# Optimization experiments

Hardware: AMD Instinct MI355X
Metric: run time of the kernel (lower is better)

## Reference

```python
import jax, jax.numpy as jnp
import numpy as np

N = 131072        # total points
M = 34            # max_num_neighbors (hard-coded in forward)
K = 15            # kernel points (torch-points3d default for 3D KPConv)
C_IN, C_OUT = 32, 64
POINT_INFLUENCE = 0.04        # prev_grid_size * sigma
KERNEL_RADIUS = 1.5 * POINT_INFLUENCE  # _INFLUENCE_TO_RADIUS * point_influence
BN_EPS = 1e-5
NEG_SLOPE = 0.2


def setup_inputs() -> dict:
    key = jax.random.key(0)
    ks = jax.random.split(key, 6)
    # points in a [0, 0.1]^3 box so random neighbors can fall inside the influence radius
    xyz = jax.random.uniform(ks[0], (N, 3), jnp.float32) * 0.1
    feats = jax.random.normal(ks[1], (N, C_IN), jnp.float32)
    neighbor_idx = jax.random.randint(ks[2], (N, M), 0, N, dtype=jnp.int32)
    # fixed kernel-point disposition: points inside a sphere of radius KERNEL_RADIUS
    kp_dir = jax.random.normal(ks[3], (K, 3), jnp.float32)
    kp_dir = kp_dir / jnp.linalg.norm(kp_dir, axis=1, keepdims=True)
    kp_rad = jax.random.uniform(ks[4], (K, 1), jnp.float32) ** (1.0 / 3.0)
    k_points = kp_dir * kp_rad * KERNEL_RADIUS
    weight = jax.random.normal(ks[5], (K, C_IN, C_OUT), jnp.float32) / np.sqrt(K * C_IN)
    gamma = jnp.ones((C_OUT,), jnp.float32)
    beta = jnp.zeros((C_OUT,), jnp.float32)
    return {"xyz": xyz, "feats": feats, "neighbor_idx": neighbor_idx,
            "weight": weight, "k_points": k_points, "gamma": gamma, "beta": beta}


def _kpconv(xyz, feats, neighbor_idx, weight, k_points):
    # shadow point / shadow feature row for out-of-range neighbor index == N
    sup = jnp.concatenate([xyz, jnp.full((1, 3), 1e6, xyz.dtype)], axis=0)
    f = jnp.concatenate([feats, jnp.zeros((1, feats.shape[1]), feats.dtype)], axis=0)
    # [N, M, 3] neighbor offsets relative to each query point
    nb = sup[neighbor_idx] - xyz[:, None, :]
    # [N, M, K] distance from each neighbor to each kernel point
    diff = nb[:, :, None, :] - k_points[None, None, :, :]
    dist = jnp.sqrt(jnp.sum(diff * diff, axis=-1))
    # linear kernel influence, 'sum' aggregation
    w = jnp.maximum(0.0, 1.0 - dist / POINT_INFLUENCE)          # [N, M, K]
    nb_f = f[neighbor_idx]                                       # [N, M, C_IN]
    wf = jnp.einsum('nmk,nmc->nkc', w, nb_f)                     # [N, K, C_IN]
    return jnp.einsum('nkc,kcd->nd', wf, weight)                 # [N, C_OUT]


def reference(xyz, feats, neighbor_idx, weight, k_points, gamma, beta):
    out = _kpconv(xyz, feats, neighbor_idx, weight, k_points)
    # FastBatchNorm1d (training-mode batch statistics) + LeakyReLU(0.2)
    mean = jnp.mean(out, axis=0)
    var = jnp.mean((out - mean) ** 2, axis=0)
    out = (out - mean) * jax.lax.rsqrt(var + BN_EPS) * gamma + beta
    return jnp.where(out >= 0, out, NEG_SLOPE * out)
```

## Files before the change

kernel.cpp:

```cpp
#include <hip/hip_runtime.h>

#define NPTS 131072
#define MNBR 34
#define KP 15
#define CIN 32
#define COUT 64
#define INV_INFL 25.0f
#define BN_EPS 1e-5f
#define NEG_SLOPE 0.2f
#define PPB 16
#define NBLK (NPTS / PPB)
#define NBIN 2048

typedef unsigned short u16;
typedef unsigned int u32;
typedef short short8 __attribute__((ext_vector_type(8)));
typedef float f32x4 __attribute__((ext_vector_type(4)));

static __device__ __forceinline__ u16 f2bf(float f) {
    u32 x = __float_as_uint(f);
    x += 0x7fffu + ((x >> 16) & 1u);
    return (u16)(x >> 16);
}
static __device__ __forceinline__ u32 pk2bf(float lo, float hi) {
    u32 a = __float_as_uint(lo) + 0x8000u;
    u32 b = __float_as_uint(hi) + 0x8000u;
    return (a >> 16) | (b & 0xffff0000u);
}

#define WS_WT   0u
#define WS_SCSH 65536u
#define WS_SP   131072u
#define WS_QP   655360u
#define WS_FB   1179648u

__global__ __launch_bounds__(256) void prep(const float* __restrict__ Wg,
                                            const float* __restrict__ feats,
                                            u16* __restrict__ WT, u32* __restrict__ FBu,
                                            float* __restrict__ SpQp) {
    int b = blockIdx.x;
    if (b < 120) {
        int tid2 = b * 256 + threadIdx.x;
        int i = tid2 >> 6, d = tid2 & 63;
        WT[d * 480 + i] = f2bf(Wg[tid2]);
    } else if (b < 120 + 8193) {
        int g = (b - 120) * 256 + threadIdx.x;
        if (g < ((NPTS + 1) * CIN) / 2) {
            int e = g * 2;
            u32 v = 0;
            if (e < NPTS * CIN)
                v = (u32)f2bf(feats[e]) | ((u32)f2bf(feats[e + 1]) << 16);
            FBu[g] = v;
        }
    } else {
        int idx = (b - 8313) * 256 + threadIdx.x;
        if (idx < 2 * 64 * NBIN) SpQp[idx] = 0.f;
    }
}

__global__ __launch_bounds__(128, 3) void kpconv_conv(
    const float* __restrict__ xyz, const int* __restrict__ nbr,
    const u16* __restrict__ FB, const u16* __restrict__ WT,
    const float* __restrict__ kpts, float* __restrict__ out,
    float* __restrict__ Sp, float* __restrict__ Qp)
{
    __shared__ u32 wf[PPB * 256];
    __shared__ u32 nbt[2][16 * 68];
    __shared__ u16 wk[2][16 * 64];

    const int tid = threadIdx.x, lane = tid & 63, wave = tid >> 6;
    const int q = lane >> 4, t = lane & 15;

    float ax[16], ay[16], az[16], ck[16];
    #pragma unroll
    for (int k = 0; k < KP; ++k) {
        float kx = kpts[3 * k], ky = kpts[3 * k + 1], kz = kpts[3 * k + 2];
        ax[k] = -2.f * kx; ay[k] = -2.f * ky; az[k] = -2.f * kz;
        ck[k] = fmaf(kx, kx, fmaf(ky, ky, kz * kz));
    }
    ax[15] = 0.f; ay[15] = 0.f; az[15] = 0.f; ck[15] = 1e12f;

    u32* nb = nbt[wave];
    u16* wl = wk[wave];
    const int pbase = blockIdx.x * PPB + wave * 8;

    int ci = NPTS;
    if (lane < MNBR) ci = nbr[(size_t)pbase * MNBR + lane];
    if ((unsigned)ci > (unsigned)NPTS) ci = NPTS;
    int nn = NPTS;
    if (lane < MNBR) nn = nbr[(size_t)(pbase + 1) * MNBR + lane];
    if ((unsigned)nn > (unsigned)NPTS) nn = NPTS;

    int il = ci < NPTS ? ci : 0;
    float cnx = xyz[3 * il], cny = xyz[3 * il + 1], cnz = xyz[3 * il + 2];
    const uint4* fr = (const uint4*)(FB + (size_t)ci * CIN);
    uint4 cf0 = fr[0], cf1 = fr[1], cf2 = fr[2], cf3 = fr[3];

    for (int p = 0; p < 8; ++p) {
        int nn2 = NPTS;
        if (p < 6) {
            if (lane < MNBR) nn2 = nbr[(size_t)(pbase + p + 2) * MNBR + lane];
            if ((unsigned)nn2 > (unsigned)NPTS) nn2 = NPTS;
        }
        float nx1 = 0.f, ny1 = 0.f, nz1 = 0.f;
        uint4 nf0 = {}, nf1 = {}, nf2 = {}, nf3 = {};
        if (p < 7) {
            int il1 = nn < NPTS ? nn : 0;
            nx1 = xyz[3 * il1]; ny1 = xyz[3 * il1 + 1]; nz1 = xyz[3 * il1 + 2];
            const uint4* fr1 = (const uint4*)(FB + (size_t)nn * CIN);
            nf0 = fr1[0]; nf1 = fr1[1]; nf2 = fr1[2]; nf3 = fr1[3];
        }

        const int n = pbase + p;
        const float qx = xyz[3 * n], qy = xyz[3 * n + 1], qz = xyz[3 * n + 2];
        float ox = cnx - qx, oy = cny - qy, oz = cnz - qz;
        if (ci >= NPTS) { ox = 1e6f; oy = 0.f; oz = 0.f; }
        const float oo = fmaf(ox, ox, fmaf(oy, oy, oz * oz));

        #pragma unroll
        for (int k = 0; k < 16; ++k) {
            float d2 = fmaf(ox, ax[k], fmaf(oy, ay[k], fmaf(oz, az[k], ck[k]))) + oo;
            float d = __builtin_amdgcn_sqrtf(d2);
            float w = fmaxf(0.f, fmaf(d, -INV_INFL, 1.f));
            wl[k * 64 + ((((lane >> 3) ^ (k & 7))) << 3) + (lane & 7)] =
                (u16)((__float_as_uint(w) + 0x8000u) >> 16);
        }

        {
            u32 fd[16] = {cf0.x, cf0.y, cf0.z, cf0.w, cf1.x, cf1.y, cf1.z, cf1.w,
                          cf2.x, cf2.y, cf2.z, cf2.w, cf3.x, cf3.y, cf3.z, cf3.w};
            #pragma unroll
            for (int w16 = 0; w16 < 16; ++w16)
                nb[w16 * 68 + lane] = fd[w16];
        }

        cnx = nx1; cny = ny1; cnz = nz1;
        cf0 = nf0; cf1 = nf1; cf2 = nf2; cf3 = nf3;
        ci = nn; nn = nn2;

        short8 a0 = *(const short8*)&wl[t * 64 + (((q) ^ (t & 7)) << 3)];
        short8 a1 = *(const short8*)&wl[t * 64 + (((4 + q) ^ (t & 7)) << 3)];

        uint4 b0 = *(const uint4*)&nb[t * 68 + 8 * q];
        uint4 b1 = *(const uint4*)&nb[t * 68 + 8 * q + 4];
        uint4 b2 = *(const uint4*)&nb[t * 68 + 8 * q + 32];
        uint4 b3 = *(const uint4*)&nb[t * 68 + 8 * q + 36];
        union { short8 v; u32 d[4]; } e0, o0, e1, o1;
        {
            u32 r0[8] = {b0.x, b0.y, b0.z, b0.w, b1.x, b1.y, b1.z, b1.w};
            u32 r1[8] = {b2.x, b2.y, b2.z, b2.w, b3.x, b3.y, b3.z, b3.w};
            #pragma unroll
            for (int i2 = 0; i2 < 4; ++i2) {
                u32 a = r0[2 * i2], b = r0[2 * i2 + 1];
                e0.d[i2] = (a & 0xffffu) | (b << 16);
                o0.d[i2] = (a >> 16) | (b & 0xffff0000u);
                a = r1[2 * i2]; b = r1[2 * i2 + 1];
                e1.d[i2] = (a & 0xffffu) | (b << 16);
                o1.d[i2] = (a >> 16) | (b & 0xffff0000u);
            }
        }

        f32x4 c0 = {0.f, 0.f, 0.f, 0.f}, c1 = {0.f, 0.f, 0.f, 0.f};
        c0 = __builtin_amdgcn_mfma_f32_16x16x32_bf16(a0, e0.v, c0, 0, 0, 0);
        c0 = __builtin_amdgcn_mfma_f32_16x16x32_bf16(a1, e1.v, c0, 0, 0, 0);
        c1 = __builtin_amdgcn_mfma_f32_16x16x32_bf16(a0, o0.v, c1, 0, 0, 0);
        c1 = __builtin_amdgcn_mfma_f32_16x16x32_bf16(a1, o1.v, c1, 0, 0, 0);

        const int row = wave * 8 + p;
        #pragma unroll
        for (int r = 0; r < 4; ++r) {
            int ko = q * 4 + r;
            u32 pk = pk2bf(c0[r], c1[r]);
            int unit = ko * 4 + (t >> 2);
            wf[row * 256 + ((unit ^ (row & 7)) << 2) + (t & 3)] = pk;
        }
    }
    __syncthreads();

    const int wcol0 = (wave * 2 + 0) * 16 + t;
    const int wcol1 = (wave * 2 + 1) * 16 + t;
    f32x4 A0 = {0.f, 0.f, 0.f, 0.f}, A1 = {0.f, 0.f, 0.f, 0.f};
    const u16* wt0 = WT + wcol0 * 480 + q * 8;
    const u16* wt1 = WT + wcol1 * 480 + q * 8;
    #pragma unroll
    for (int ks = 0; ks < KP; ++ks) {
        const int u = ks * 4 + q;
        short8 a  = *(const short8*)&wf[t * 256 + ((u ^ (t & 7)) << 2)];
        short8 bb0 = *(const short8*)(wt0 + ks * 32);
        short8 bb1 = *(const short8*)(wt1 + ks * 32);
        A0 = __builtin_amdgcn_mfma_f32_16x16x32_bf16(a, bb0, A0, 0, 0, 0);
        A1 = __builtin_amdgcn_mfma_f32_16x16x32_bf16(a, bb1, A1, 0, 0, 0);
    }
    const int base = blockIdx.x * PPB;
    float s0 = 0.f, q0 = 0.f, s1 = 0.f, q1 = 0.f;
    #pragma unroll
    for (int r = 0; r < 4; ++r) {
        float v0 = A0[r], v1 = A1[r];
        out[(base + q * 4 + r) * COUT + wcol0] = v0;
        out[(base + q * 4 + r) * COUT + wcol1] = v1;
        s0 += v0; q0 = fmaf(v0, v0, q0);
        s1 += v1; q1 = fmaf(v1, v1, q1);
    }
    s0 += __shfl_xor(s0, 16, 64); s0 += __shfl_xor(s0, 32, 64);
    q0 += __shfl_xor(q0, 16, 64); q0 += __shfl_xor(q0, 32, 64);
    s1 += __shfl_xor(s1, 16, 64); s1 += __shfl_xor(s1, 32, 64);
    q1 += __shfl_xor(q1, 16, 64); q1 += __shfl_xor(q1, 32, 64);
    if (q == 0) {
        const int bin = blockIdx.x >> 2;
        atomicAdd(&Sp[wcol0 * NBIN + bin], s0);
        atomicAdd(&Qp[wcol0 * NBIN + bin], q0);
        atomicAdd(&Sp[wcol1 * NBIN + bin], s1);
        atomicAdd(&Qp[wcol1 * NBIN + bin], q1);
    }
}

__global__ __launch_bounds__(256) void bn_reduce(
    const float* __restrict__ Sp, const float* __restrict__ Qp,
    const float* __restrict__ gamma, const float* __restrict__ beta,
    float* __restrict__ scsh)
{
    const int ch = blockIdx.x;
    const float4* S4 = (const float4*)(Sp + ch * NBIN);
    const float4* Q4 = (const float4*)(Qp + ch * NBIN);
    float s = 0.f, qq = 0.f;
    #pragma unroll
    for (int r = 0; r < NBIN / 4 / 256; ++r) {
        float4 a = S4[threadIdx.x + 256 * r]; s  += a.x + a.y + a.z + a.w;
        float4 b = Q4[threadIdx.x + 256 * r]; qq += b.x + b.y + b.z + b.w;
    }
    #pragma unroll
    for (int off = 1; off < 64; off <<= 1) {
        s += __shfl_xor(s, off, 64); qq += __shfl_xor(qq, off, 64);
    }
    __shared__ float red[8];
    const int w = threadIdx.x >> 6;
    if ((threadIdx.x & 63) == 0) { red[w * 2] = s; red[w * 2 + 1] = qq; }
    __syncthreads();
    if (threadIdx.x == 0) {
        s  = red[0] + red[2] + red[4] + red[6];
        qq = red[1] + red[3] + red[5] + red[7];
        float mean = s * (1.0f / NPTS);
        float var  = qq * (1.0f / NPTS) - mean * mean;
        float sc = gamma[ch] * rsqrtf(var + BN_EPS);
        scsh[ch] = sc;
        scsh[64 + ch] = beta[ch] - mean * sc;
    }
}

__global__ __launch_bounds__(256) void bn_apply(
    float* __restrict__ out, const float* __restrict__ scsh)
{
    __shared__ float sc[64], sh[64];
    const int tid = threadIdx.x;
    if (tid < 64) { sc[tid] = scsh[tid]; sh[tid] = scsh[64 + tid]; }
    __syncthreads();
    const int gid = blockIdx.x * 256 + tid;
    float4 v = ((const float4*)out)[gid];
    const int c0 = (gid * 4) & 63;
    float y0 = fmaf(v.x, sc[c0 + 0], sh[c0 + 0]);
    float y1 = fmaf(v.y, sc[c0 + 1], sh[c0 + 1]);
    float y2 = fmaf(v.z, sc[c0 + 2], sh[c0 + 2]);
    float y3 = fmaf(v.w, sc[c0 + 3], sh[c0 + 3]);
    float4 w;
    w.x = fmaxf(y0, NEG_SLOPE * y0);
    w.y = fmaxf(y1, NEG_SLOPE * y1);
    w.z = fmaxf(y2, NEG_SLOPE * y2);
    w.w = fmaxf(y3, NEG_SLOPE * y3);
    ((float4*)out)[gid] = w;
}

extern "C" void kernel_launch(void* const* d_in, const int* in_sizes, int n_in,
                              void* d_out, int out_size, void* d_ws, size_t ws_size,
                              hipStream_t stream) {
    (void)in_sizes; (void)n_in; (void)out_size; (void)ws_size;
    const float* xyz   = (const float*)d_in[0];
    const float* feats = (const float*)d_in[1];
    const int*   nbr   = (const int*)d_in[2];
    const float* Wg    = (const float*)d_in[3];
    const float* kpts  = (const float*)d_in[4];
    const float* gamma = (const float*)d_in[5];
    const float* beta  = (const float*)d_in[6];
    float* out = (float*)d_out;
    char* ws = (char*)d_ws;
    u16*   WT   = (u16*)(ws + WS_WT);
    float* scsh = (float*)(ws + WS_SCSH);
    float* Sp   = (float*)(ws + WS_SP);
    float* Qp   = (float*)(ws + WS_QP);
    u16*   FB   = (u16*)(ws + WS_FB);

    prep<<<dim3(120 + 8193 + 1024), dim3(256), 0, stream>>>(Wg, feats, WT, (u32*)FB, Sp);
    kpconv_conv<<<dim3(NBLK), dim3(128), 0, stream>>>(xyz, nbr, FB, WT, kpts, out, Sp, Qp);
    bn_reduce<<<dim3(64), dim3(256), 0, stream>>>(Sp, Qp, gamma, beta, scsh);
    bn_apply<<<dim3((NPTS * COUT) / (256 * 4)), dim3(256), 0, stream>>>(out, scsh);
}
```

Baseline: 248.0 us.

## Restructure neighbor gather and kernel-weight compute to avoid LDS transposes

Adds a padded float4 xyz table built in prep. The conv kernel now has each lane gather one 64-byte feature column slice per neighbor row directly into MFMA operand layout, which removes the per-lane 16-dword LDS write and transpose of neighbor features. Kernel-point weights are computed per lane for one kernel point t over 8 neighbors straight into registers, using a second mostly-zero MFMA for neighbors 32-33, instead of writing a 16x64 weight tile to LDS. It also shrinks the BN partial-sum bins from 2048 to 512, which puts more atomics on each bin. The gathers become narrower (4-byte loads per lane), which may change memory efficiency.

```diff
diff --git a/kernel.cpp b/kernel.cpp
--- a/kernel.cpp
+++ b/kernel.cpp
@@ -10,7 +10,7 @@
 #define NEG_SLOPE 0.2f
 #define PPB 16
 #define NBLK (NPTS / PPB)
-#define NBIN 2048
+#define NBIN 512
 
 typedef unsigned short u16;
 typedef unsigned int u32;
@@ -31,20 +31,29 @@
 #define WS_WT   0u
 #define WS_SCSH 65536u
 #define WS_SP   131072u
-#define WS_QP   655360u
-#define WS_FB   1179648u
+#define WS_QP   262144u
+#define WS_XY   393216u
+#define WS_FB   2490624u
 
 __global__ __launch_bounds__(256) void prep(const float* __restrict__ Wg,
                                             const float* __restrict__ feats,
-                                            u16* __restrict__ WT, u32* __restrict__ FBu,
-                                            float* __restrict__ SpQp) {
+                                            const float* __restrict__ xyz,
+                                            u16* __restrict__ WT, float4* __restrict__ XY,
+                                            u32* __restrict__ FBu, float* __restrict__ SpQp) {
     int b = blockIdx.x;
     if (b < 120) {
-        int tid2 = b * 256 + threadIdx.x;
-        int i = tid2 >> 6, d = tid2 & 63;
-        WT[d * 480 + i] = f2bf(Wg[tid2]);
-    } else if (b < 120 + 8193) {
-        int g = (b - 120) * 256 + threadIdx.x;
+        int i2 = b * 256 + threadIdx.x;
+        WT[(i2 & 63) * 480 + (i2 >> 6)] = f2bf(Wg[i2]);
+    } else if (b < 633) {
+        int r = (b - 120) * 256 + threadIdx.x;
+        if (r <= NPTS) {
+            float4 v;
+            if (r < NPTS) v = make_float4(xyz[3 * r], xyz[3 * r + 1], xyz[3 * r + 2], 0.f);
+            else          v = make_float4(1e6f, 1e6f, 1e6f, 0.f);
+            XY[r] = v;
+        }
+    } else if (b < 8826) {
+        int g = (b - 633) * 256 + threadIdx.x;
         if (g < ((NPTS + 1) * CIN) / 2) {
             int e = g * 2;
             u32 v = 0;
@@ -53,118 +62,125 @@
             FBu[g] = v;
         }
     } else {
-        int idx = (b - 8313) * 256 + threadIdx.x;
-        if (idx < 2 * 64 * NBIN) SpQp[idx] = 0.f;
+        SpQp[(b - 8826) * 256 + threadIdx.x] = 0.f;
     }
 }
 
 __global__ __launch_bounds__(128, 3) void kpconv_conv(
     const float* __restrict__ xyz, const int* __restrict__ nbr,
-    const u16* __restrict__ FB, const u16* __restrict__ WT,
-    const float* __restrict__ kpts, float* __restrict__ out,
-    float* __restrict__ Sp, float* __restrict__ Qp)
+    const float4* __restrict__ XY, const u32* __restrict__ FBu,
+    const u16* __restrict__ WT, const float* __restrict__ kpts,
+    float* __restrict__ out, float* __restrict__ Sp, float* __restrict__ Qp)
 {
     __shared__ u32 wf[PPB * 256];
-    __shared__ u32 nbt[2][16 * 68];
-    __shared__ u16 wk[2][16 * 64];
+    __shared__ float4 offs4[2][2][64];
+    __shared__ u32 idxs[2][2][64];
 
     const int tid = threadIdx.x, lane = tid & 63, wave = tid >> 6;
     const int q = lane >> 4, t = lane & 15;
-
-    float ax[16], ay[16], az[16], ck[16];
-    #pragma unroll
-    for (int k = 0; k < KP; ++k) {
-        float kx = kpts[3 * k], ky = kpts[3 * k + 1], kz = kpts[3 * k + 2];
-        ax[k] = -2.f * kx; ay[k] = -2.f * ky; az[k] = -2.f * kz;
-        ck[k] = fmaf(kx, kx, fmaf(ky, ky, kz * kz));
-    }
-    ax[15] = 0.f; ay[15] = 0.f; az[15] = 0.f; ck[15] = 1e12f;
-
-    u32* nb = nbt[wave];
-    u16* wl = wk[wave];
     const int pbase = blockIdx.x * PPB + wave * 8;
 
-    int ci = NPTS;
-    if (lane < MNBR) ci = nbr[(size_t)pbase * MNBR + lane];
-    if ((unsigned)ci > (unsigned)NPTS) ci = NPTS;
-    int nn = NPTS;
-    if (lane < MNBR) nn = nbr[(size_t)(pbase + 1) * MNBR + lane];
-    if ((unsigned)nn > (unsigned)NPTS) nn = NPTS;
-
-    int il = ci < NPTS ? ci : 0;
-    float cnx = xyz[3 * il], cny = xyz[3 * il + 1], cnz = xyz[3 * il + 2];
-    const uint4* fr = (const uint4*)(FB + (size_t)ci * CIN);
-    uint4 cf0 = fr[0], cf1 = fr[1], cf2 = fr[2], cf3 = fr[3];
+    float axt = 0.f, ayt = 0.f, azt = 0.f, ckt = 1e30f;
+    if (t < KP) {
+        float kx = kpts[3 * t], ky = kpts[3 * t + 1], kz = kpts[3 * t + 2];
+        axt = -2.f * kx; ayt = -2.f * ky; azt = -2.f * kz;
+        ckt = fmaf(kx, kx, fmaf(ky, ky, kz * kz));
+    }
+    const int wslot = (lane & ~7) | ((lane ^ (lane >> 3)) & 7);
+
+    auto ldnbr = [&](int pp) {
+        int v = NPTS;
+        if (lane < MNBR) v = nbr[(size_t)(pbase + pp) * MNBR + lane];
+        if ((u32)v > (u32)NPTS) v = NPTS;
+        return v;
+    };
+
+    u32 fbC[8], fbN[8] = {0,0,0,0,0,0,0,0};
+    u32 d32C = 0, d33C = 0, d32N = 0, d33N = 0;
+
+    int ixA = ldnbr(0);
+    int ix1 = ldnbr(1);
+    int ix2 = ldnbr(2);
+    float4 pn0 = XY[ixA];
+    float4 pn1 = XY[ix1];
+    {
+        const int n1 = pbase;
+        float qx = xyz[3 * n1], qy = xyz[3 * n1 + 1], qz = xyz[3 * n1 + 2];
+        float ox = pn0.x - qx, oy = pn0.y - qy, oz = pn0.z - qz;
+        offs4[wave][0][wslot] = make_float4(ox, oy, oz, fmaf(ox, ox, fmaf(oy, oy, oz * oz)));
+        idxs[wave][0][lane] = (u32)ixA;
+        #pragma unroll
+        for (int j = 0; j < 8; ++j) {
+            u32 row = idxs[wave][0][q * 8 + j];
+            fbC[j] = FBu[(size_t)row * 16 + t];
+        }
+        int r32 = __builtin_amdgcn_readlane(ixA, 32);
+        int r33 = __builtin_amdgcn_readlane(ixA, 33);
+        d32C = FBu[(size_t)r32 * 16 + t];
+        d33C = FBu[(size_t)r33 * 16 + t];
+    }
 
     for (int p = 0; p < 8; ++p) {
-        int nn2 = NPTS;
-        if (p < 6) {
-            if (lane < MNBR) nn2 = nbr[(size_t)(pbase + p + 2) * MNBR + lane];
-            if ((unsigned)nn2 > (unsigned)NPTS) nn2 = NPTS;
-        }
-        float nx1 = 0.f, ny1 = 0.f, nz1 = 0.f;
-        uint4 nf0 = {}, nf1 = {}, nf2 = {}, nf3 = {};
+        int ixN = NPTS;
+        if (p < 5) ixN = ldnbr(p + 3);
+        float4 pn2 = make_float4(1e6f, 1e6f, 1e6f, 0.f);
+        if (p < 6) pn2 = XY[ix2];
         if (p < 7) {
-            int il1 = nn < NPTS ? nn : 0;
-            nx1 = xyz[3 * il1]; ny1 = xyz[3 * il1 + 1]; nz1 = xyz[3 * il1 + 2];
-            const uint4* fr1 = (const uint4*)(FB + (size_t)nn * CIN);
-            nf0 = fr1[0]; nf1 = fr1[1]; nf2 = fr1[2]; nf3 = fr1[3];
-        }
-
-        const int n = pbase + p;
-        const float qx = xyz[3 * n], qy = xyz[3 * n + 1], qz = xyz[3 * n + 2];
-        float ox = cnx - qx, oy = cny - qy, oz = cnz - qz;
-        if (ci >= NPTS) { ox = 1e6f; oy = 0.f; oz = 0.f; }
-        const float oo = fmaf(ox, ox, fmaf(oy, oy, oz * oz));
-
-        #pragma unroll
-        for (int k = 0; k < 16; ++k) {
-            float d2 = fmaf(ox, ax[k], fmaf(oy, ay[k], fmaf(oz, az[k], ck[k]))) + oo;
-            float d = __builtin_amdgcn_sqrtf(d2);
-            float w = fmaxf(0.f, fmaf(d, -INV_INFL, 1.f));
-            wl[k * 64 + ((((lane >> 3) ^ (k & 7))) << 3) + (lane & 7)] =
-                (u16)((__float_as_uint(w) + 0x8000u) >> 16);
-        }
-
+            const int n1 = pbase + p + 1;
+            float qx = xyz[3 * n1], qy = xyz[3 * n1 + 1], qz = xyz[3 * n1 + 2];
+            float ox = pn1.x - qx, oy = pn1.y - qy, oz = pn1.z - qz;
+            const int bb = (p + 1) & 1;
+            offs4[wave][bb][wslot] = make_float4(ox, oy, oz, fmaf(ox, ox, fmaf(oy, oy, oz * oz)));
+            idxs[wave][bb][lane] = (u32)ix1;
+            #pragma unroll
+            for (int j = 0; j < 8; ++j) {
+                u32 row = idxs[wave][bb][q * 8 + j];
+                fbN[j] = FBu[(size_t)row * 16 + t];
+            }
+            int r32 = __builtin_amdgcn_readlane(ix1, 32);
+            int r33 = __builtin_amdgcn_readlane(ix1, 33);
+            d32N = FBu[(size_t)r32 * 16 + t];
+            d33N = FBu[(size_t)r33 * 16 + t];
+        }
+
+        const float4* ob = &offs4[wave][p & 1][0];
+        float wj[8];
+        #pragma unroll
+        for (int j = 0; j < 8; ++j) {
+            float4 o = ob[q * 8 + (j ^ q)];
+            float d2 = fmaf(o.x, axt, fmaf(o.y, ayt, fmaf(o.z, azt, ckt))) + o.w;
+            float dd = __builtin_amdgcn_sqrtf(d2);
+            wj[j] = fmaxf(0.f, fmaf(dd, -INV_INFL, 1.f));
+        }
+        union { short8 v; u32 d[4]; } a1, a2, e1, o1, e2, o2;
+        #pragma unroll
+        for (int i = 0; i < 4; ++i) a1.d[i] = pk2bf(wj[2 * i], wj[2 * i + 1]);
         {
-            u32 fd[16] = {cf0.x, cf0.y, cf0.z, cf0.w, cf1.x, cf1.y, cf1.z, cf1.w,
-                          cf2.x, cf2.y, cf2.z, cf2.w, cf3.x, cf3.y, cf3.z, cf3.w};
-            #pragma unroll
-            for (int w16 = 0; w16 < 16; ++w16)
-                nb[w16 * 68 + lane] = fd[w16];
-        }
-
-        cnx = nx1; cny = ny1; cnz = nz1;
-        cf0 = nf0; cf1 = nf1; cf2 = nf2; cf3 = nf3;
-        ci = nn; nn = nn2;
-
-        short8 a0 = *(const short8*)&wl[t * 64 + (((q) ^ (t & 7)) << 3)];
-        short8 a1 = *(const short8*)&wl[t * 64 + (((4 + q) ^ (t & 7)) << 3)];
-
-        uint4 b0 = *(const uint4*)&nb[t * 68 + 8 * q];
-        uint4 b1 = *(const uint4*)&nb[t * 68 + 8 * q + 4];
-        uint4 b2 = *(const uint4*)&nb[t * 68 + 8 * q + 32];
-        uint4 b3 = *(const uint4*)&nb[t * 68 + 8 * q + 36];
-        union { short8 v; u32 d[4]; } e0, o0, e1, o1;
+            float4 oA = ob[36], oB = ob[37];
+            float dA = __builtin_amdgcn_sqrtf(fmaf(oA.x, axt, fmaf(oA.y, ayt, fmaf(oA.z, azt, ckt))) + oA.w);
+            float dB = __builtin_amdgcn_sqrtf(fmaf(oB.x, axt, fmaf(oB.y, ayt, fmaf(oB.z, azt, ckt))) + oB.w);
+            float wA = fmaxf(0.f, fmaf(dA, -INV_INFL, 1.f));
+            float wB = fmaxf(0.f, fmaf(dB, -INV_INFL, 1.f));
+            a2.d[0] = (q == 0) ? pk2bf(wA, wB) : 0u;
+            a2.d[1] = 0; a2.d[2] = 0; a2.d[3] = 0;
+        }
+        #pragma unroll
+        for (int i = 0; i < 4; ++i) {
+            u32 aa = fbC[2 * i], bb2 = fbC[2 * i + 1];
+            e1.d[i] = (aa & 0xffffu) | (bb2 << 16);
+            o1.d[i] = (aa >> 16) | (bb2 & 0xffff0000u);
+        }
         {
-            u32 r0[8] = {b0.x, b0.y, b0.z, b0.w, b1.x, b1.y, b1.z, b1.w};
-            u32 r1[8] = {b2.x, b2.y, b2.z, b2.w, b3.x, b3.y, b3.z, b3.w};
-            #pragma unroll
-            for (int i2 = 0; i2 < 4; ++i2) {
-                u32 a = r0[2 * i2], b = r0[2 * i2 + 1];
-                e0.d[i2] = (a & 0xffffu) | (b << 16);
-                o0.d[i2] = (a >> 16) | (b & 0xffff0000u);
-                a = r1[2 * i2]; b = r1[2 * i2 + 1];
-                e1.d[i2] = (a & 0xffffu) | (b << 16);
-                o1.d[i2] = (a >> 16) | (b & 0xffff0000u);
-            }
-        }
-
+            u32 lo = (d32C & 0xffffu) | (d33C << 16);
+            u32 hi = (d32C >> 16) | (d33C & 0xffff0000u);
+            e2.d[0] = (q == 0) ? lo : 0u;  e2.d[1] = 0; e2.d[2] = 0; e2.d[3] = 0;
+            o2.d[0] = (q == 0) ? hi : 0u;  o2.d[1] = 0; o2.d[2] = 0; o2.d[3] = 0;
+        }
         f32x4 c0 = {0.f, 0.f, 0.f, 0.f}, c1 = {0.f, 0.f, 0.f, 0.f};
-        c0 = __builtin_amdgcn_mfma_f32_16x16x32_bf16(a0, e0.v, c0, 0, 0, 0);
-        c0 = __builtin_amdgcn_mfma_f32_16x16x32_bf16(a1, e1.v, c0, 0, 0, 0);
-        c1 = __builtin_amdgcn_mfma_f32_16x16x32_bf16(a0, o0.v, c1, 0, 0, 0);
-        c1 = __builtin_amdgcn_mfma_f32_16x16x32_bf16(a1, o1.v, c1, 0, 0, 0);
+        c0 = __builtin_amdgcn_mfma_f32_16x16x32_bf16(a1.v, e1.v, c0, 0, 0, 0);
+        c0 = __builtin_amdgcn_mfma_f32_16x16x32_bf16(a2.v, e2.v, c0, 0, 0, 0);
+        c1 = __builtin_amdgcn_mfma_f32_16x16x32_bf16(a1.v, o1.v, c1, 0, 0, 0);
+        c1 = __builtin_amdgcn_mfma_f32_16x16x32_bf16(a2.v, o2.v, c1, 0, 0, 0);
 
         const int row = wave * 8 + p;
         #pragma unroll
@@ -174,6 +190,11 @@
             int unit = ko * 4 + (t >> 2);
             wf[row * 256 + ((unit ^ (row & 7)) << 2) + (t & 3)] = pk;
         }
+
+        #pragma unroll
+        for (int j = 0; j < 8; ++j) fbC[j] = fbN[j];
+        d32C = d32N; d33C = d33N;
+        pn1 = pn2; ix1 = ix2; ix2 = ixN;
     }
     __syncthreads();
 
@@ -185,7 +206,7 @@
     #pragma unroll
     for (int ks = 0; ks < KP; ++ks) {
         const int u = ks * 4 + q;
-        short8 a  = *(const short8*)&wf[t * 256 + ((u ^ (t & 7)) << 2)];
+        short8 a   = *(const short8*)&wf[t * 256 + ((u ^ (t & 7)) << 2)];
         short8 bb0 = *(const short8*)(wt0 + ks * 32);
         short8 bb1 = *(const short8*)(wt1 + ks * 32);
         A0 = __builtin_amdgcn_mfma_f32_16x16x32_bf16(a, bb0, A0, 0, 0, 0);
@@ -206,7 +227,7 @@
     s1 += __shfl_xor(s1, 16, 64); s1 += __shfl_xor(s1, 32, 64);
     q1 += __shfl_xor(q1, 16, 64); q1 += __shfl_xor(q1, 32, 64);
     if (q == 0) {
-        const int bin = blockIdx.x >> 2;
+        const int bin = blockIdx.x >> 4;
         atomicAdd(&Sp[wcol0 * NBIN + bin], s0);
         atomicAdd(&Qp[wcol0 * NBIN + bin], q0);
         atomicAdd(&Sp[wcol1 * NBIN + bin], s1);
@@ -220,23 +241,21 @@
     float* __restrict__ scsh)
 {
     const int ch = blockIdx.x;
-    const float4* S4 = (const float4*)(Sp + ch * NBIN);
-    const float4* Q4 = (const float4*)(Qp + ch * NBIN);
+    const int tid = threadIdx.x;
     float s = 0.f, qq = 0.f;
-    #pragma unroll
-    for (int r = 0; r < NBIN / 4 / 256; ++r) {
-        float4 a = S4[threadIdx.x + 256 * r]; s  += a.x + a.y + a.z + a.w;
-        float4 b = Q4[threadIdx.x + 256 * r]; qq += b.x + b.y + b.z + b.w;
+    if (tid < NBIN / 4) {
+        float4 a = ((const float4*)(Sp + ch * NBIN))[tid]; s  = a.x + a.y + a.z + a.w;
+        float4 b = ((const float4*)(Qp + ch * NBIN))[tid]; qq = b.x + b.y + b.z + b.w;
     }
     #pragma unroll
     for (int off = 1; off < 64; off <<= 1) {
         s += __shfl_xor(s, off, 64); qq += __shfl_xor(qq, off, 64);
     }
     __shared__ float red[8];
-    const int w = threadIdx.x >> 6;
-    if ((threadIdx.x & 63) == 0) { red[w * 2] = s; red[w * 2 + 1] = qq; }
+    const int w = tid >> 6;
+    if ((tid & 63) == 0) { red[w * 2] = s; red[w * 2 + 1] = qq; }
     __syncthreads();
-    if (threadIdx.x == 0) {
+    if (tid == 0) {
         s  = red[0] + red[2] + red[4] + red[6];
         qq = red[1] + red[3] + red[5] + red[7];
         float mean = s * (1.0f / NPTS);
@@ -282,14 +301,15 @@
     const float* beta  = (const float*)d_in[6];
     float* out = (float*)d_out;
     char* ws = (char*)d_ws;
-    u16*   WT   = (u16*)(ws + WS_WT);
-    float* scsh = (float*)(ws + WS_SCSH);
-    float* Sp   = (float*)(ws + WS_SP);
-    float* Qp   = (float*)(ws + WS_QP);
-    u16*   FB   = (u16*)(ws + WS_FB);
-
-    prep<<<dim3(120 + 8193 + 1024), dim3(256), 0, stream>>>(Wg, feats, WT, (u32*)FB, Sp);
-    kpconv_conv<<<dim3(NBLK), dim3(128), 0, stream>>>(xyz, nbr, FB, WT, kpts, out, Sp, Qp);
+    u16*    WT   = (u16*)(ws + WS_WT);
+    float*  scsh = (float*)(ws + WS_SCSH);
+    float*  Sp   = (float*)(ws + WS_SP);
+    float*  Qp   = (float*)(ws + WS_QP);
+    float4* XY   = (float4*)(ws + WS_XY);
+    u32*    FBu  = (u32*)(ws + WS_FB);
+
+    prep<<<dim3(9082), dim3(256), 0, stream>>>(Wg, feats, xyz, WT, XY, FBu, Sp);
+    kpconv_conv<<<dim3(NBLK), dim3(128), 0, stream>>>(xyz, nbr, XY, FBu, WT, kpts, out, Sp, Qp);
     bn_reduce<<<dim3(64), dim3(256), 0, stream>>>(Sp, Qp, gamma, beta, scsh);
     bn_apply<<<dim3((NPTS * COUT) / (256 * 4)), dim3(256), 0, stream>>>(out, scsh);
 }
```

New measurement: 219.9 us. 1.13x faster.
